# Performance work log

Hardware: AMD Instinct MI355X
Metric: run time of the kernel (lower is better)

Reference implementation:

```python
import jax, jax.numpy as jnp
import numpy as np

B, F_C, F_F = 2, 32768, 131072
C_IN, C_OUT, W_DIM, COLOR = 128, 64, 512, 3
K2 = 9
PAD0, PAD1 = 192, 384
ACT_GAIN = float(np.sqrt(2.0))  # lrelu def_gain


def _gather(x, nbr, is_pad, pad):
    # x: [N, C]; nbr: [M, k] indices into [N + pad]; is_pad: [M, k] bool
    padded = jnp.concatenate([x, jnp.zeros((pad, x.shape[1]), x.dtype)], 0)
    g = padded[nbr]  # [M, k, C]
    return jnp.where(is_pad[..., None], jnp.zeros((), x.dtype), g)


def _affine(w, aw, ab):
    # StyleGAN FullyConnectedLayer: runtime weight gain 1/sqrt(fan_in), bias_init=1
    return w @ (aw.T * (1.0 / np.sqrt(aw.shape[1]))) + ab


def _modconv(xg, weight, styles, demodulate=True):
    # xg: [N, k, I]; weight: [O, I, 1, k]; styles: [B, I]
    n, k, ci = xg.shape
    w = weight[:, :, 0, :][None, :, :, :] * styles[:, None, :, None]  # [B,O,I,k]
    if demodulate:
        w = w * jax.lax.rsqrt(jnp.sum(w * w, axis=(2, 3), keepdims=True) + 1e-8)
    xb = xg.reshape(styles.shape[0], -1, k, ci)  # [B,F,k,I]
    return jnp.einsum('bfki,boik->bfo', xb, w).reshape(n, -1)


def _smooth_upsample(x, nbr, is_pad, pad, pool_map):
    # upsample coarse->fine via parent map, then masked neighborhood mean
    xf = x[pool_map]  # [N_fine, C]
    g = _gather(xf, nbr, is_pad, pad)  # [N_fine, k, C]
    cnt = jnp.maximum(jnp.sum(~is_pad, axis=1), 1).astype(x.dtype)
    return jnp.sum(g, axis=1) / cnt[:, None]


def _act(x, gain):
    # clamp_gain(lrelu(x), act_gain*gain, 256*gain)
    y = jnp.where(x >= 0, x, 0.2 * x)
    return jnp.clip(y * (ACT_GAIN * gain), -256.0 * gain, 256.0 * gain)


def setup_inputs():
    key = jax.random.key(0)
    ks = jax.random.split(key, 16)
    x = jax.random.normal(ks[0], (B * F_C, C_IN), jnp.float32)
    img = jax.random.normal(ks[1], (B * F_C, COLOR), jnp.float32)
    ws = jax.random.normal(ks[2], (B, 3, W_DIM), jnp.float32)
    fn0 = jax.random.randint(ks[3], (B * F_C, K2), 0, B * F_C + PAD0, jnp.int32)
    fn1 = jax.random.randint(ks[4], (B * F_F, K2), 0, B * F_F + PAD1, jnp.int32)
    fip0 = jax.random.bernoulli(ks[5], 0.05, (B * F_C, K2))
    fip1 = jax.random.bernoulli(ks[6], 0.05, (B * F_F, K2))
    pool_map0 = jax.random.randint(ks[7], (B * F_F,), 0, B * F_C, jnp.int32)
    a0_w = jax.random.normal(ks[8], (C_IN, W_DIM), jnp.float32)
    a0_b = jnp.ones((C_IN,), jnp.float32)
    W0 = jax.random.normal(ks[9], (C_OUT, C_IN, 1, K2), jnp.float32)
    b0 = jnp.zeros((C_OUT,), jnp.float32)
    ns0 = jnp.zeros((1,), jnp.float32)
    nc0 = jax.random.normal(ks[10], (F_F,), jnp.float32)
    a1_w = jax.random.normal(ks[11], (C_OUT, W_DIM), jnp.float32)
    a1_b = jnp.ones((C_OUT,), jnp.float32)
    W1 = jax.random.normal(ks[12], (C_OUT, C_OUT, 1, K2), jnp.float32)
    b1 = jnp.zeros((C_OUT,), jnp.float32)
    ns1 = jnp.zeros((1,), jnp.float32)
    nc1 = jax.random.normal(ks[13], (F_F,), jnp.float32)
    at_w = jax.random.normal(ks[14], (C_OUT, W_DIM), jnp.float32)
    at_b = jnp.ones((C_OUT,), jnp.float32)
    Wt = jax.random.normal(ks[15], (COLOR, C_OUT, 1, 1), jnp.float32)
    bt = jnp.zeros((COLOR,), jnp.float32)
    return {"x": x, "img": img, "ws": ws, "a0_w": a0_w, "a0_b": a0_b, "W0": W0,
            "b0": b0, "ns0": ns0, "nc0": nc0, "a1_w": a1_w, "a1_b": a1_b,
            "W1": W1, "b1": b1, "ns1": ns1, "nc1": nc1, "at_w": at_w,
            "at_b": at_b, "Wt": Wt, "bt": bt, "fn0": fn0, "fip0": fip0,
            "fn1": fn1, "fip1": fip1, "pool_map0": pool_map0,
            "pad0": PAD0, "pad1": PAD1}


def reference(x, img, ws, a0_w, a0_b, W0, b0, ns0, nc0, a1_w, a1_b, W1, b1, ns1,
              nc1, at_w, at_b, Wt, bt, fn0, fip0, fn1, fip1, pool_map0, pad0, pad1):
    b = ws.shape[0]
    w0, w1, w2 = ws[:, 0], ws[:, 1], ws[:, 2]
    # conv0: coarse gather -> mod conv -> smooth upsample to fine -> noise/bias/act
    s0 = _affine(w0, a0_w, a0_b)
    noise0 = jnp.tile(nc0[None, :], (b, 1)).reshape(-1, 1) * ns0  # noise_mode='const'
    h = _modconv(_gather(x, fn0, fip0, pad0), W0, s0)
    h = _smooth_upsample(h, fn1, fip1, pad1, pool_map0)
    h = _act(h + noise0 + b0[None, :], 1.0)
    # conv1: fine level, no resampler
    s1 = _affine(w1, a1_w, a1_b)
    noise1 = jnp.tile(nc1[None, :], (b, 1)).reshape(-1, 1) * ns1
    h = _modconv(_gather(h, fn1, fip1, pad1), W1, s1)
    h = _act(h + noise1 + b1[None, :], 1.0)
    # torgb: kernel_size=1 -> self index only, no demodulation
    st = _affine(w2, at_w, at_b) * (1.0 / np.sqrt(C_OUT))
    y = _modconv(_gather(h, fn1[:, :1], fip1[:, :1], pad1), Wt, st, demodulate=False)
    y = jnp.clip(y + bt[None, :], -256.0, 256.0)
    img = _smooth_upsample(img, fn1, fip1, pad1, pool_map0) + y
    return (h, img)
```

## Files before the change

### kernel.cpp

```cpp
#include <hip/hip_runtime.h>
#include <hip/hip_bf16.h>

constexpr int F_C   = 32768;
constexpr int F_F   = 131072;
constexpr int N0    = 65536;
constexpr int N1    = 262144;
constexpr int C_IN  = 128;
constexpr int W_DIM = 512;
constexpr int K2c   = 9;
constexpr float RS512     = 0.04419417382415922f;
constexpr float ACT_GAINc = 1.4142135623730951f;

constexpr size_t FO_S0  = 0;
constexpr size_t FO_S1  = 256;
constexpr size_t FO_ST  = 384;
constexpr size_t OFF_WM0T = 2048;
constexpr size_t OFF_WM1T = OFF_WM0T + 294912;
constexpr size_t OFF_H0   = 458752;
constexpr size_t OFF_HA   = OFF_H0 + (size_t)8388608;
constexpr size_t OFF_YPRE = OFF_H0;
constexpr size_t OFF_XB   = OFF_HA;

typedef short s16x8 __attribute__((ext_vector_type(8)));
typedef float f32x4 __attribute__((ext_vector_type(4)));

__device__ __forceinline__ float b2f(unsigned short u) {
    union { unsigned int i; float f; } v; v.i = ((unsigned int)u) << 16; return v.f;
}
__device__ __forceinline__ unsigned short f2b(float f) {
    __hip_bfloat16 h = __float2bfloat16(f);
    return *reinterpret_cast<unsigned short*>(&h);
}
__device__ __forceinline__ float waveRedSum(float v) {
    for (int m = 32; m; m >>= 1) v += __shfl_xor(v, m, 64);
    return v;
}
__device__ __forceinline__ float actf(float v) {
    float y = (v >= 0.f) ? v : 0.2f * v;
    y *= ACT_GAINc;
    return fminf(fmaxf(y, -256.f), 256.f);
}

__global__ __launch_bounds__(64)
void k_styles(const float* __restrict__ wsF,
              const float* __restrict__ a0w, const float* __restrict__ a0b,
              const float* __restrict__ a1w, const float* __restrict__ a1b,
              const float* __restrict__ atw, const float* __restrict__ atb,
              float* __restrict__ fr)
{
    int bid = blockIdx.x, lane = threadIdx.x;
    int bb, ii, ll, row; const float *aw, *ab; float* dst; float post = 1.f;
    if (bid < 256)      { bb = bid >> 7;             ii = bid & 127; ll = 0; aw = a0w; ab = a0b; dst = fr + FO_S0; row = 128; }
    else if (bid < 384) { int t = bid - 256; bb = t >> 6; ii = t & 63; ll = 1; aw = a1w; ab = a1b; dst = fr + FO_S1; row = 64; }
    else                { int t = bid - 384; bb = t >> 6; ii = t & 63; ll = 2; aw = atw; ab = atb; dst = fr + FO_ST; row = 64; post = 0.125f; }
    const float* wsv = wsF + (size_t)(bb * 3 + ll) * W_DIM;
    const float* awr = aw + (size_t)ii * W_DIM;
    float s = 0.f;
    for (int j = lane; j < W_DIM; j += 64) s += wsv[j] * awr[j];
    s = waveRedSum(s);
    if (lane == 0) dst[bb * row + ii] = (s * RS512 + ab[ii]) * post;
}

__global__ __launch_bounds__(256)
void k_wmod(const float* __restrict__ W0,
            const float* __restrict__ W1,
            const float* __restrict__ fr,
            unsigned short* __restrict__ wm0T,
            unsigned short* __restrict__ wm1T)
{
    int bo = blockIdx.x, tid = threadIdx.x;
    int b, o, CI, NE; const float* W; const float* S; unsigned short* dst;
    if (bo < 128) { b = bo >> 6; o = bo & 63; CI = 128; NE = 1152; W = W0; S = fr + FO_S0; dst = wm0T; }
    else { int t = bo - 128; b = t >> 6; o = t & 63; CI = 64; NE = 576; W = W1; S = fr + FO_S1; dst = wm1T; }
    const float* Wo = W + (size_t)o * NE;
    const float* Sb = S + (size_t)b * CI;
    float ss = 0.f;
    for (int idx = tid; idx < NE; idx += 256) {
        int i = idx / K2c;
        float p = Wo[idx] * Sb[i];
        ss += p * p;
    }
    __shared__ float red[4];
    float s = waveRedSum(ss);
    if ((tid & 63) == 0) red[tid >> 6] = s;
    __syncthreads();
    float d = rsqrtf(red[0] + red[1] + red[2] + red[3] + 1e-8f);
    for (int idx = tid; idx < NE; idx += 256) {
        int i = idx / K2c, kk = idx - i * K2c;
        dst[((size_t)(b * K2c + kk) * 64 + o) * CI + i] = f2b(Wo[idx] * Sb[i] * d);
    }
}

__global__ __launch_bounds__(256)
void k_xcvt(const float* __restrict__ xF, unsigned short* __restrict__ xB)
{
    int i = blockIdx.x * 256 + threadIdx.x;
    float4 f = ((const float4*)xF)[i];
    union { unsigned short u[4]; uint2 v; } t;
    t.u[0] = f2b(f.x); t.u[1] = f2b(f.y); t.u[2] = f2b(f.z); t.u[3] = f2b(f.w);
    ((uint2*)xB)[i] = t.v;
}

__global__ __launch_bounds__(256, 2)
void k_layer0(const unsigned short* __restrict__ xB,
              const int*  __restrict__ fn0,
              const int*  __restrict__ fip0,
              const unsigned short* __restrict__ wm0T,
              unsigned short* __restrict__ h0B)
{
    __shared__ unsigned short W_lds[9 * 4096];
    const int tid  = threadIdx.x;
    const int g0   = blockIdx.x * 256;
    const int b    = g0 / F_C;
    const int wave = tid >> 6, lane = tid & 63;
    const int lg   = lane >> 4, lr = lane & 15;
    const int wbase = g0 + wave * 64;
    const unsigned short* wtap = wm0T + (size_t)b * K2c * 64 * C_IN;

    int nbrk[4][9];
    #pragma unroll
    for (int rg = 0; rg < 4; ++rg) {
        int row = wbase + rg * 16 + lr;
        #pragma unroll
        for (int k = 0; k < 9; ++k) {
            int fn = fn0[(size_t)row * 9 + k];
            int ip = fip0[(size_t)row * 9 + k];
            nbrk[rg][k] = (!ip && fn < N0) ? fn : -1;
        }
    }

    f32x4 acc[4][4] = {};
    for (int h = 0; h < 2; ++h) {
        __syncthreads();
        #pragma unroll
        for (int t = 0; t < 18; ++t) {
            int idx = tid + 256 * t;
            int tap = idx >> 9;
            int rem = idx & 511;
            int row = rem >> 3, cc = rem & 7;
            uint4 v = *(const uint4*)(wtap + ((size_t)tap * 64 + row) * C_IN + h * 64 + cc * 8);
            *(uint4*)(&W_lds[tap * 4096 + row * 64 + ((cc ^ (row & 7)) << 3)]) = v;
        }
        __syncthreads();
        #pragma unroll
        for (int kk = 0; kk < 9; ++kk) {
            s16x8 bf[2][4];
            #pragma unroll
            for (int c2 = 0; c2 < 2; ++c2)
                #pragma unroll
                for (int nt = 0; nt < 4; ++nt) {
                    int row = nt * 16 + lr;
                    bf[c2][nt] = *(const s16x8*)(&W_lds[kk * 4096 + row * 64 + (((c2 * 4 + lg) ^ (row & 7)) << 3)]);
                }
            #pragma unroll
            for (int rg = 0; rg < 4; ++rg) {
                int nbr = nbrk[rg][kk];
                int pc  = nbr >= 0 ? nbr : 0;
                const uint4* ap = (const uint4*)(xB + (size_t)pc * C_IN) + lg;
                uint4 a0 = ap[h * 8];
                uint4 a1 = ap[h * 8 + 4];
                if (nbr < 0) { a0 = uint4{0,0,0,0}; a1 = uint4{0,0,0,0}; }
                s16x8 af0 = *reinterpret_cast<const s16x8*>(&a0);
                s16x8 af1 = *reinterpret_cast<const s16x8*>(&a1);
                #pragma unroll
                for (int nt = 0; nt < 4; ++nt)
                    acc[rg][nt] = __builtin_amdgcn_mfma_f32_16x16x32_bf16(af0, bf[0][nt], acc[rg][nt], 0, 0, 0);
                #pragma unroll
                for (int nt = 0; nt < 4; ++nt)
                    acc[rg][nt] = __builtin_amdgcn_mfma_f32_16x16x32_bf16(af1, bf[1][nt], acc[rg][nt], 0, 0, 0);
            }
        }
    }
    #pragma unroll
    for (int rg = 0; rg < 4; ++rg)
        #pragma unroll
        for (int nt = 0; nt < 4; ++nt) {
            int o = nt * 16 + lr;
            #pragma unroll
            for (int r = 0; r < 4; ++r) {
                int node = wbase + rg * 16 + lg * 4 + r;
                h0B[(size_t)node * 64 + o] = f2b(acc[rg][nt][r]);
            }
        }
}

__global__ __launch_bounds__(256)
void k_ha(const unsigned short* __restrict__ h0B,
          const int*  __restrict__ fn1,
          const int*  __restrict__ fip1,
          const int*  __restrict__ pool,
          const float* __restrict__ nc0,
          const float* __restrict__ ns0,
          const float* __restrict__ b0,
          const float* __restrict__ imgF,
          unsigned short* __restrict__ haB,
          float* __restrict__ outImg)
{
    __shared__ int   pmArr[288];
    __shared__ int   vArr[288];
    __shared__ float invCnt[32];
    const int tid = threadIdx.x;
    const int n0  = blockIdx.x * 32;
    for (int idx = tid; idx < 288; idx += 256) {
        int fn = fn1[(size_t)n0 * K2c + idx];
        int ip = fip1[(size_t)n0 * K2c + idx];
        int v  = !ip;
        int pm = -1;
        if (v && fn < N1) pm = pool[fn];
        pmArr[idx] = pm;
        vArr[idx]  = v;
    }
    __syncthreads();
    if (tid < 32) {
        int c = 0;
        #pragma unroll
        for (int k = 0; k < K2c; ++k) c += vArr[tid * K2c + k];
        invCnt[tid] = 1.f / (float)(c > 0 ? c : 1);
    }
    __syncthreads();
    if (tid < 96) {
        int node = tid / 3, c = tid - node * 3;
        float s = 0.f;
        #pragma unroll
        for (int k = 0; k < K2c; ++k) {
            int pm = pmArr[node * K2c + k];
            int pc = pm >= 0 ? pm : 0;
            float m = pm >= 0 ? 1.f : 0.f;
            s += m * imgF[(size_t)pc * 3 + c];
        }
        outImg[(size_t)(n0 + node) * 3 + c] = s * invCnt[node];
    }
    const int node = tid >> 3;
    const int cg   = tid & 7;
    const int g    = n0 + node;
    float s[8] = {};
    #pragma unroll
    for (int k = 0; k < K2c; ++k) {
        int pm = pmArr[node * K2c + k];
        int pc = pm >= 0 ? pm : 0;
        uint4 v = *(const uint4*)(h0B + (size_t)pc * 64 + cg * 8);
        float m = pm >= 0 ? 1.f : 0.f;
        const unsigned short* u = (const unsigned short*)&v;
        #pragma unroll
        for (int j = 0; j < 8; ++j) s[j] += m * b2f(u[j]);
    }
    const float ic  = invCnt[node];
    const float nz  = nc0[g & (F_F - 1)] * ns0[0];
    unsigned short outv[8];
    #pragma unroll
    for (int j = 0; j < 8; ++j) {
        float v = s[j] * ic + nz + b0[cg * 8 + j];
        outv[j] = f2b(actf(v));
    }
    *(uint4*)(haB + (size_t)g * 64 + cg * 8) = *(const uint4*)outv;
}

__global__ __launch_bounds__(256, 2)
void k_layer1(const unsigned short* __restrict__ haB,
              const int*  __restrict__ fn1,
              const int*  __restrict__ fip1,
              const unsigned short* __restrict__ wm1T,
              const float* __restrict__ nc1,
              const float* __restrict__ ns1,
              const float* __restrict__ b1,
              const float* __restrict__ stS,
              const float* __restrict__ WtF,
              float* __restrict__ hOut,
              float* __restrict__ yPre2)
{
    __shared__ unsigned short W_lds[9 * 4096];
    const int tid  = threadIdx.x;
    const int g0   = blockIdx.x * 256;
    const int b    = g0 / F_F;
    const int wave = tid >> 6, lane = tid & 63;
    const int lg   = lane >> 4, lr = lane & 15;
    const int wbase = g0 + wave * 64;
    const unsigned short* wtap = wm1T + (size_t)b * K2c * 4096;

    #pragma unroll
    for (int t = 0; t < 18; ++t) {
        int idx = tid + 256 * t;
        int tap = idx >> 9;
        int rem = idx & 511;
        int row = rem >> 3, c = rem & 7;
        uint4 v = ((const uint4*)wtap)[idx];
        *(uint4*)(&W_lds[tap * 4096 + row * 64 + ((c ^ (row & 7)) << 3)]) = v;
    }

    int nbrk[4][9];
    #pragma unroll
    for (int rg = 0; rg < 4; ++rg) {
        int row = wbase + rg * 16 + lr;
        #pragma unroll
        for (int k = 0; k < 9; ++k) {
            int fn = fn1[(size_t)row * 9 + k];
            int ip = fip1[(size_t)row * 9 + k];
            nbrk[rg][k] = (!ip && fn < N1) ? fn : -1;
        }
    }

    uint4 pa[2][4][2];
    #pragma unroll
    for (int kk = 0; kk < 2; ++kk)
        #pragma unroll
        for (int rg = 0; rg < 4; ++rg) {
            int nbr = nbrk[rg][kk];
            int pc  = nbr >= 0 ? nbr : 0;
            const uint4* ap = (const uint4*)(haB + (size_t)pc * 64) + lg;
            pa[kk][rg][0] = ap[0];
            pa[kk][rg][1] = ap[4];
        }

    __syncthreads();

    f32x4 acc[4][4] = {};
    #pragma unroll
    for (int kk = 0; kk < 9; ++kk) {
        const int slot = kk & 1;
        s16x8 bf[2][4];
        #pragma unroll
        for (int h = 0; h < 2; ++h)
            #pragma unroll
            for (int nt = 0; nt < 4; ++nt) {
                int row = nt * 16 + lr;
                bf[h][nt] = *(const s16x8*)(&W_lds[kk * 4096 + row * 64 + (((h * 4 + lg) ^ (row & 7)) << 3)]);
            }
        uint4 cur[4][2];
        #pragma unroll
        for (int rg = 0; rg < 4; ++rg) {
            cur[rg][0] = pa[slot][rg][0];
            cur[rg][1] = pa[slot][rg][1];
        }
        if (kk + 2 < 9) {
            #pragma unroll
            for (int rg = 0; rg < 4; ++rg) {
                int nbr = nbrk[rg][kk + 2];
                int pc  = nbr >= 0 ? nbr : 0;
                const uint4* ap = (const uint4*)(haB + (size_t)pc * 64) + lg;
                pa[slot][rg][0] = ap[0];
                pa[slot][rg][1] = ap[4];
            }
        }
        #pragma unroll
        for (int rg = 0; rg < 4; ++rg) {
            int nbr = nbrk[rg][kk];
            uint4 a0 = cur[rg][0], a1 = cur[rg][1];
            if (nbr < 0) { a0 = uint4{0,0,0,0}; a1 = uint4{0,0,0,0}; }
            s16x8 af0 = *reinterpret_cast<const s16x8*>(&a0);
            s16x8 af1 = *reinterpret_cast<const s16x8*>(&a1);
            #pragma unroll
            for (int nt = 0; nt < 4; ++nt)
                acc[rg][nt] = __builtin_amdgcn_mfma_f32_16x16x32_bf16(af0, bf[0][nt], acc[rg][nt], 0, 0, 0);
            #pragma unroll
            for (int nt = 0; nt < 4; ++nt)
                acc[rg][nt] = __builtin_amdgcn_mfma_f32_16x16x32_bf16(af1, bf[1][nt], acc[rg][nt], 0, 0, 0);
        }
    }

    const float nsc = ns1[0];
    #pragma unroll
    for (int rg = 0; rg < 4; ++rg) {
        float p00[4] = {}, p01[4] = {}, p02[4] = {};
        float p10[4] = {}, p11[4] = {}, p12[4] = {};
        #pragma unroll
        for (int nt = 0; nt < 4; ++nt) {
            int o = nt * 16 + lr;
            float bias = b1[o];
            float st0  = stS[o], st1 = stS[64 + o];
            float wt0 = WtF[o], wt1 = WtF[64 + o], wt2 = WtF[128 + o];
            float w00 = wt0 * st0, w01 = wt1 * st0, w02 = wt2 * st0;
            float w10 = wt0 * st1, w11 = wt1 * st1, w12 = wt2 * st1;
            #pragma unroll
            for (int r = 0; r < 4; ++r) {
                int node = wbase + rg * 16 + lg * 4 + r;
                float v  = actf(acc[rg][nt][r] + nc1[node & (F_F - 1)] * nsc + bias);
                hOut[(size_t)node * 64 + o] = v;
                p00[r] += v * w00; p01[r] += v * w01; p02[r] += v * w02;
                p10[r] += v * w10; p11[r] += v * w11; p12[r] += v * w12;
            }
        }
        #pragma unroll
        for (int m = 1; m < 16; m <<= 1) {
            #pragma unroll
            for (int r = 0; r < 4; ++r) {
                p00[r] += __shfl_xor(p00[r], m, 64);
                p01[r] += __shfl_xor(p01[r], m, 64);
                p02[r] += __shfl_xor(p02[r], m, 64);
                p10[r] += __shfl_xor(p10[r], m, 64);
                p11[r] += __shfl_xor(p11[r], m, 64);
                p12[r] += __shfl_xor(p12[r], m, 64);
            }
        }
        if (lr == 0) {
            #pragma unroll
            for (int r = 0; r < 4; ++r) {
                int node = wbase + rg * 16 + lg * 4 + r;
                yPre2[(size_t)node * 6 + 0] = p00[r];
                yPre2[(size_t)node * 6 + 1] = p01[r];
                yPre2[(size_t)node * 6 + 2] = p02[r];
                yPre2[(size_t)node * 6 + 3] = p10[r];
                yPre2[(size_t)node * 6 + 4] = p11[r];
                yPre2[(size_t)node * 6 + 5] = p12[r];
            }
        }
    }
}

__global__ __launch_bounds__(256)
void k_rgb(const float* __restrict__ yPre2,
           const int*  __restrict__ fn1,
           const int*  __restrict__ fip1,
           const float* __restrict__ btF,
           float* __restrict__ outImg)
{
    const int n = blockIdx.x * 256 + threadIdx.x;
    const int bOut = n / F_F;
    int fn0 = fn1[(size_t)n * K2c];
    int ip0 = fip1[(size_t)n * K2c];
    int nb0 = (!ip0 && fn0 < N1) ? fn0 : -1;
    float y0 = 0.f, y1 = 0.f, y2 = 0.f;
    if (nb0 >= 0) {
        const float* yp = yPre2 + (size_t)nb0 * 6 + bOut * 3;
        y0 = yp[0]; y1 = yp[1]; y2 = yp[2];
    }
    y0 = fminf(fmaxf(y0 + btF[0], -256.f), 256.f);
    y1 = fminf(fmaxf(y1 + btF[1], -256.f), 256.f);
    y2 = fminf(fmaxf(y2 + btF[2], -256.f), 256.f);
    outImg[(size_t)n * 3 + 0] += y0;
    outImg[(size_t)n * 3 + 1] += y1;
    outImg[(size_t)n * 3 + 2] += y2;
}

extern "C" void kernel_launch(void* const* d_in, const int* in_sizes, int n_in,
                              void* d_out, int out_size, void* d_ws, size_t ws_size,
                              hipStream_t stream)
{
    const float* xF   = (const float*)d_in[0];
    const float* imgF = (const float*)d_in[1];
    const float* wsF  = (const float*)d_in[2];
    const float* a0w  = (const float*)d_in[3];
    const float* a0b  = (const float*)d_in[4];
    const float* W0w  = (const float*)d_in[5];
    const float* b0w  = (const float*)d_in[6];
    const float* ns0  = (const float*)d_in[7];
    const float* nc0  = (const float*)d_in[8];
    const float* a1w  = (const float*)d_in[9];
    const float* a1b  = (const float*)d_in[10];
    const float* W1w  = (const float*)d_in[11];
    const float* b1w  = (const float*)d_in[12];
    const float* ns1  = (const float*)d_in[13];
    const float* nc1  = (const float*)d_in[14];
    const float* atw  = (const float*)d_in[15];
    const float* atb  = (const float*)d_in[16];
    const float* WtF  = (const float*)d_in[17];
    const float* btF  = (const float*)d_in[18];
    const int* fn0  = (const int*)d_in[19];
    const int* fip0 = (const int*)d_in[20];
    const int* fn1  = (const int*)d_in[21];
    const int* fip1 = (const int*)d_in[22];
    const int* pool = (const int*)d_in[23];

    char* wsb = (char*)d_ws;
    float* fr = (float*)wsb;
    unsigned short* wm0T = (unsigned short*)(wsb + OFF_WM0T);
    unsigned short* wm1T = (unsigned short*)(wsb + OFF_WM1T);
    unsigned short* h0B  = (unsigned short*)(wsb + OFF_H0);
    unsigned short* haB  = (unsigned short*)(wsb + OFF_HA);
    unsigned short* xB   = (unsigned short*)(wsb + OFF_XB);
    float* yPre2         = (float*)(wsb + OFF_YPRE);

    float* hOut   = (float*)d_out;
    float* imgOut = hOut + (size_t)N1 * 64;

    hipLaunchKernelGGL(k_styles, dim3(512), dim3(64), 0, stream,
                       wsF, a0w, a0b, a1w, a1b, atw, atb, fr);
    hipLaunchKernelGGL(k_wmod, dim3(256), dim3(256), 0, stream,
                       W0w, W1w, fr, wm0T, wm1T);
    hipLaunchKernelGGL(k_xcvt, dim3((N0 * C_IN) / 4 / 256), dim3(256), 0, stream,
                       xF, xB);
    hipLaunchKernelGGL(k_layer0, dim3(N0 / 256), dim3(256), 0, stream,
                       xB, fn0, fip0, wm0T, h0B);
    hipLaunchKernelGGL(k_ha, dim3(N1 / 32), dim3(256), 0, stream,
                       h0B, fn1, fip1, pool, nc0, ns0, b0w, imgF, haB, imgOut);
    hipLaunchKernelGGL(k_layer1, dim3(N1 / 256), dim3(256), 0, stream,
                       haB, fn1, fip1, wm1T, nc1, ns1, b1w,
                       fr + FO_ST, WtF, hOut, yPre2);
    hipLaunchKernelGGL(k_rgb, dim3(N1 / 256), dim3(256), 0, stream,
                       yPre2, fn1, fip1, btF, imgOut);
}
```

Measured before the change: 183.6 us.

## Fuse style, weight-modulation and input-conversion kernels; precompute self-neighbor index for RGB

Merges the style affine, weight modulation/demodulation, and fp32-to-bf16 input conversion into one launch. Each modulation block now recomputes its own style vector serially per thread instead of reading one precomputed by a separate kernel. The smooth-upsample kernel also writes a compact per-node self-neighbor index, so the final RGB kernel no longer does strided reads of fn1 and fip1. This removes two launches and some strided traffic, at the cost of redundant serial dot products in the prep blocks.

```diff
diff --git a/kernel.cpp b/kernel.cpp
--- a/kernel.cpp
+++ b/kernel.cpp
@@ -11,8 +11,6 @@
 constexpr float RS512     = 0.04419417382415922f;
 constexpr float ACT_GAINc = 1.4142135623730951f;
 
-constexpr size_t FO_S0  = 0;
-constexpr size_t FO_S1  = 256;
 constexpr size_t FO_ST  = 384;
 constexpr size_t OFF_WM0T = 2048;
 constexpr size_t OFF_WM1T = OFF_WM0T + 294912;
@@ -20,6 +18,7 @@
 constexpr size_t OFF_HA   = OFF_H0 + (size_t)8388608;
 constexpr size_t OFF_YPRE = OFF_H0;
 constexpr size_t OFF_XB   = OFF_HA;
+constexpr size_t OFF_NB0  = OFF_HA + (size_t)33554432;
 
 typedef short s16x8 __attribute__((ext_vector_type(8)));
 typedef float f32x4 __attribute__((ext_vector_type(4)));
@@ -41,43 +40,55 @@
     return fminf(fmaxf(y, -256.f), 256.f);
 }
 
-__global__ __launch_bounds__(64)
-void k_styles(const float* __restrict__ wsF,
-              const float* __restrict__ a0w, const float* __restrict__ a0b,
-              const float* __restrict__ a1w, const float* __restrict__ a1b,
-              const float* __restrict__ atw, const float* __restrict__ atb,
-              float* __restrict__ fr)
-{
-    int bid = blockIdx.x, lane = threadIdx.x;
-    int bb, ii, ll, row; const float *aw, *ab; float* dst; float post = 1.f;
-    if (bid < 256)      { bb = bid >> 7;             ii = bid & 127; ll = 0; aw = a0w; ab = a0b; dst = fr + FO_S0; row = 128; }
-    else if (bid < 384) { int t = bid - 256; bb = t >> 6; ii = t & 63; ll = 1; aw = a1w; ab = a1b; dst = fr + FO_S1; row = 64; }
-    else                { int t = bid - 384; bb = t >> 6; ii = t & 63; ll = 2; aw = atw; ab = atb; dst = fr + FO_ST; row = 64; post = 0.125f; }
-    const float* wsv = wsF + (size_t)(bb * 3 + ll) * W_DIM;
-    const float* awr = aw + (size_t)ii * W_DIM;
-    float s = 0.f;
-    for (int j = lane; j < W_DIM; j += 64) s += wsv[j] * awr[j];
-    s = waveRedSum(s);
-    if (lane == 0) dst[bb * row + ii] = (s * RS512 + ab[ii]) * post;
-}
-
 __global__ __launch_bounds__(256)
-void k_wmod(const float* __restrict__ W0,
-            const float* __restrict__ W1,
-            const float* __restrict__ fr,
+void k_prep(const float* __restrict__ wsF,
+            const float* __restrict__ a0w, const float* __restrict__ a0b,
+            const float* __restrict__ a1w, const float* __restrict__ a1b,
+            const float* __restrict__ atw, const float* __restrict__ atb,
+            const float* __restrict__ W0,  const float* __restrict__ W1,
+            const float* __restrict__ xF,
+            float* __restrict__ fr,
             unsigned short* __restrict__ wm0T,
-            unsigned short* __restrict__ wm1T)
-{
-    int bo = blockIdx.x, tid = threadIdx.x;
-    int b, o, CI, NE; const float* W; const float* S; unsigned short* dst;
-    if (bo < 128) { b = bo >> 6; o = bo & 63; CI = 128; NE = 1152; W = W0; S = fr + FO_S0; dst = wm0T; }
-    else { int t = bo - 128; b = t >> 6; o = t & 63; CI = 64; NE = 576; W = W1; S = fr + FO_S1; dst = wm1T; }
+            unsigned short* __restrict__ wm1T,
+            unsigned short* __restrict__ xB)
+{
+    const int bo = blockIdx.x, tid = threadIdx.x;
+    if (bo >= 258) {
+        int i = (bo - 258) * 256 + tid;
+        float4 f = ((const float4*)xF)[i];
+        union { unsigned short u[4]; uint2 v; } t;
+        t.u[0] = f2b(f.x); t.u[1] = f2b(f.y); t.u[2] = f2b(f.z); t.u[3] = f2b(f.w);
+        ((uint2*)xB)[i] = t.v;
+        return;
+    }
+    if (bo >= 256) {
+        int b = bo - 256;
+        if (tid < 64) {
+            const float* wsv = wsF + (size_t)(b * 3 + 2) * W_DIM;
+            const float* awr = atw + (size_t)tid * W_DIM;
+            float s = 0.f;
+            for (int j = 0; j < W_DIM; ++j) s += wsv[j] * awr[j];
+            fr[FO_ST + b * 64 + tid] = (s * RS512 + atb[tid]) * 0.125f;
+        }
+        return;
+    }
+    int b, o, CI, NE, ll; const float* W; const float* aw; const float* ab; unsigned short* dst;
+    if (bo < 128) { b = bo >> 6; o = bo & 63; CI = 128; NE = 1152; ll = 0; W = W0; aw = a0w; ab = a0b; dst = wm0T; }
+    else { int t = bo - 128; b = t >> 6; o = t & 63; CI = 64; NE = 576; ll = 1; W = W1; aw = a1w; ab = a1b; dst = wm1T; }
+    __shared__ float sS[128];
+    if (tid < CI) {
+        const float* wsv = wsF + (size_t)(b * 3 + ll) * W_DIM;
+        const float* awr = aw + (size_t)tid * W_DIM;
+        float s = 0.f;
+        for (int j = 0; j < W_DIM; ++j) s += wsv[j] * awr[j];
+        sS[tid] = s * RS512 + ab[tid];
+    }
+    __syncthreads();
     const float* Wo = W + (size_t)o * NE;
-    const float* Sb = S + (size_t)b * CI;
     float ss = 0.f;
     for (int idx = tid; idx < NE; idx += 256) {
         int i = idx / K2c;
-        float p = Wo[idx] * Sb[i];
+        float p = Wo[idx] * sS[i];
         ss += p * p;
     }
     __shared__ float red[4];
@@ -87,18 +98,8 @@
     float d = rsqrtf(red[0] + red[1] + red[2] + red[3] + 1e-8f);
     for (int idx = tid; idx < NE; idx += 256) {
         int i = idx / K2c, kk = idx - i * K2c;
-        dst[((size_t)(b * K2c + kk) * 64 + o) * CI + i] = f2b(Wo[idx] * Sb[i] * d);
-    }
-}
-
-__global__ __launch_bounds__(256)
-void k_xcvt(const float* __restrict__ xF, unsigned short* __restrict__ xB)
-{
-    int i = blockIdx.x * 256 + threadIdx.x;
-    float4 f = ((const float4*)xF)[i];
-    union { unsigned short u[4]; uint2 v; } t;
-    t.u[0] = f2b(f.x); t.u[1] = f2b(f.y); t.u[2] = f2b(f.z); t.u[3] = f2b(f.w);
-    ((uint2*)xB)[i] = t.v;
+        dst[((size_t)(b * K2c + kk) * 64 + o) * CI + i] = f2b(Wo[idx] * sS[i] * d);
+    }
 }
 
 __global__ __launch_bounds__(256, 2)
@@ -194,7 +195,8 @@
           const float* __restrict__ b0,
           const float* __restrict__ imgF,
           unsigned short* __restrict__ haB,
-          float* __restrict__ outImg)
+          float* __restrict__ outImg,
+          int* __restrict__ nb0T)
 {
     __shared__ int   pmArr[288];
     __shared__ int   vArr[288];
@@ -209,6 +211,8 @@
         if (v && fn < N1) pm = pool[fn];
         pmArr[idx] = pm;
         vArr[idx]  = v;
+        int nd = idx / K2c;
+        if (idx - nd * K2c == 0) nb0T[n0 + nd] = (v && fn < N1) ? fn : -1;
     }
     __syncthreads();
     if (tid < 32) {
@@ -408,16 +412,13 @@
 
 __global__ __launch_bounds__(256)
 void k_rgb(const float* __restrict__ yPre2,
-           const int*  __restrict__ fn1,
-           const int*  __restrict__ fip1,
+           const int*  __restrict__ nb0T,
            const float* __restrict__ btF,
            float* __restrict__ outImg)
 {
     const int n = blockIdx.x * 256 + threadIdx.x;
     const int bOut = n / F_F;
-    int fn0 = fn1[(size_t)n * K2c];
-    int ip0 = fip1[(size_t)n * K2c];
-    int nb0 = (!ip0 && fn0 < N1) ? fn0 : -1;
+    int nb0 = nb0T[n];
     float y0 = 0.f, y1 = 0.f, y2 = 0.f;
     if (nb0 >= 0) {
         const float* yp = yPre2 + (size_t)nb0 * 6 + bOut * 3;
@@ -468,23 +469,21 @@
     unsigned short* haB  = (unsigned short*)(wsb + OFF_HA);
     unsigned short* xB   = (unsigned short*)(wsb + OFF_XB);
     float* yPre2         = (float*)(wsb + OFF_YPRE);
+    int*   nb0T          = (int*)(wsb + OFF_NB0);
 
     float* hOut   = (float*)d_out;
     float* imgOut = hOut + (size_t)N1 * 64;
 
-    hipLaunchKernelGGL(k_styles, dim3(512), dim3(64), 0, stream,
-                       wsF, a0w, a0b, a1w, a1b, atw, atb, fr);
-    hipLaunchKernelGGL(k_wmod, dim3(256), dim3(256), 0, stream,
-                       W0w, W1w, fr, wm0T, wm1T);
-    hipLaunchKernelGGL(k_xcvt, dim3((N0 * C_IN) / 4 / 256), dim3(256), 0, stream,
-                       xF, xB);
+    hipLaunchKernelGGL(k_prep, dim3(258 + (N0 * C_IN) / 4 / 256), dim3(256), 0, stream,
+                       wsF, a0w, a0b, a1w, a1b, atw, atb, W0w, W1w, xF,
+                       fr, wm0T, wm1T, xB);
     hipLaunchKernelGGL(k_layer0, dim3(N0 / 256), dim3(256), 0, stream,
                        xB, fn0, fip0, wm0T, h0B);
     hipLaunchKernelGGL(k_ha, dim3(N1 / 32), dim3(256), 0, stream,
-                       h0B, fn1, fip1, pool, nc0, ns0, b0w, imgF, haB, imgOut);
+                       h0B, fn1, fip1, pool, nc0, ns0, b0w, imgF, haB, imgOut, nb0T);
     hipLaunchKernelGGL(k_layer1, dim3(N1 / 256), dim3(256), 0, stream,
                        haB, fn1, fip1, wm1T, nc1, ns1, b1w,
                        fr + FO_ST, WtF, hOut, yPre2);
     hipLaunchKernelGGL(k_rgb, dim3(N1 / 256), dim3(256), 0, stream,
-                       yPre2, fn1, fip1, btF, imgOut);
-}
+                       yPre2, nb0T, btF, imgOut);
+}
```

Result: no change. 184.3 us (+0.4%).
